# Kernel tuning notes

Measured on AMD Instinct MI355X. Metric: run time of the kernel, lower is better.

The kernel has to match this reference:

```python
import jax, jax.numpy as jnp
import numpy as np
import math

D_MODEL = 1024
NUM_HEADS = 16
D_K = D_MODEL // NUM_HEADS
B, S = 2, 2048


def _linear_weight(key, out_f, in_f):
    return jax.random.normal(key, (out_f, in_f), jnp.float32) * math.sqrt(2.0 / in_f)


def setup_inputs() -> dict:
    key = jax.random.key(0)
    ks = jax.random.split(key, 5)
    x = jax.random.normal(ks[0], (B, S, D_MODEL), jnp.float32)
    return {
        "x": x,
        "Wq": _linear_weight(ks[1], D_MODEL, D_MODEL),
        "bq": jnp.zeros((D_MODEL,), jnp.float32),
        "Wk": _linear_weight(ks[2], D_MODEL, D_MODEL),
        "bk": jnp.zeros((D_MODEL,), jnp.float32),
        "Wv": _linear_weight(ks[3], D_MODEL, D_MODEL),
        "bv": jnp.zeros((D_MODEL,), jnp.float32),
        "Wo": _linear_weight(ks[4], D_MODEL, D_MODEL),
        "bo": jnp.zeros((D_MODEL,), jnp.float32),
    }


def reference(x, Wq, bq, Wk, bk, Wv, bv, Wo, bo):
    b, s, _ = x.shape
    # Projections: x @ W.T + b (CustomLinear stores weight as (out, in))
    q = jnp.einsum("bsd,ed->bse", x, Wq) + bq
    k = jnp.einsum("bsd,ed->bse", x, Wk) + bk
    v = jnp.einsum("bsd,ed->bse", x, Wv) + bv
    # (b, h, s, d_k)
    q = q.reshape(b, s, NUM_HEADS, D_K).transpose(0, 2, 1, 3)
    k = k.reshape(b, s, NUM_HEADS, D_K).transpose(0, 2, 1, 3)
    v = v.reshape(b, s, NUM_HEADS, D_K).transpose(0, 2, 1, 3)
    # Scaled dot-product attention with fully materialized scores (faithful)
    scores = jnp.einsum("bhqd,bhkd->bhqk", q, k) / math.sqrt(D_K)
    attn = jax.nn.softmax(scores, axis=-1)
    out = jnp.einsum("bhqk,bhkd->bhqd", attn, v)
    out = out.transpose(0, 2, 1, 3).reshape(b, s, D_MODEL)
    return jnp.einsum("bsd,ed->bse", out, Wo) + bo
```

## Files before the change

kernel.cpp:

```cpp
#include <hip/hip_runtime.h>
#include <hip/hip_bf16.h>

using bf16 = __hip_bfloat16;
typedef __attribute__((ext_vector_type(8))) short short8;
typedef __attribute__((ext_vector_type(4))) short s4v;
typedef __attribute__((ext_vector_type(4))) float float4v;
typedef __attribute__((ext_vector_type(4))) float f32x4;

#define MFMA16(a, b, c) __builtin_amdgcn_mfma_f32_16x16x32_bf16((a), (b), (c), 0, 0, 0)

#define GLD_LDS16(g, l)                                            \
    __builtin_amdgcn_global_load_lds(                              \
        (const __attribute__((address_space(1))) void*)(g),        \
        (__attribute__((address_space(3))) void*)(l), 16, 0, 0)

constexpr int Bc = 2;
constexpr int Sc = 2048;
constexpr int Hc = 16;
constexpr int DKc = 64;
constexpr int Dc = 1024;
constexpr size_t MEG = 1024 * 1024;

union BFU { bf16 h; short s; };

__device__ inline short bfbits(float f) {
    BFU u; u.h = __float2bfloat16(f); return u.s;
}

__device__ inline short8 load_cvt8(const float* __restrict__ p) {
    f32x4 a = *(const f32x4*)p;
    f32x4 b = *(const f32x4*)(p + 4);
    short8 r;
    r[0] = bfbits(a[0]); r[1] = bfbits(a[1]); r[2] = bfbits(a[2]); r[3] = bfbits(a[3]);
    r[4] = bfbits(b[0]); r[5] = bfbits(b[1]); r[6] = bfbits(b[2]); r[7] = bfbits(b[3]);
    return r;
}

__global__ __launch_bounds__(256) void cvt_kernel(
    const float* __restrict__ x, const float* __restrict__ Wq,
    const float* __restrict__ Wk, const float* __restrict__ Wv,
    const float* __restrict__ Wo, bf16* __restrict__ dst)
{
    const size_t i = ((size_t)blockIdx.x * 256 + threadIdx.x) * 8;
    const float* s;
    if      (i < 4 * MEG) s = x  + i;
    else if (i < 5 * MEG) s = Wq + (i - 4 * MEG);
    else if (i < 6 * MEG) s = Wk + (i - 5 * MEG);
    else if (i < 7 * MEG) s = Wv + (i - 6 * MEG);
    else                  s = Wo + (i - 7 * MEG);
    *(short8*)(dst + i) = load_cvt8(s);
}

__global__ __launch_bounds__(256) void qkv_gemm_kernel(
    const bf16* __restrict__ x,
    const bf16* __restrict__ Wq, const float* __restrict__ bq,
    const bf16* __restrict__ Wk, const float* __restrict__ bk,
    const bf16* __restrict__ Wv, const float* __restrict__ bv,
    bf16* __restrict__ q_ws, bf16* __restrict__ k_ws, bf16* __restrict__ v_ws)
{
    constexpr int BM = 128, BN = 128, BK = 32;
    __shared__ __align__(16) bf16 sA[BM * BK];
    __shared__ __align__(16) bf16 sB[BN * BK];

    const int bx = blockIdx.x;
    const int sel = bx >> 3;
    const int n0 = (bx & 7) * BN;
    const int m0 = blockIdx.y * BM;

    const bf16* __restrict__ Wsel = (sel == 0) ? Wq : ((sel == 1) ? Wk : Wv);
    const float* __restrict__ bsel = (sel == 0) ? bq : ((sel == 1) ? bk : bv);

    const int t = threadIdx.x;
    const int lane = t & 63;
    const int wave = t >> 6;
    const int ln = lane & 15;
    const int qd = lane >> 4;
    const int wm = (wave >> 1) * 64;
    const int wn = (wave & 1) * 64;

    const int gr = lane >> 2;
    const int gc = (lane & 3) * 8;

    float4v acc[4][4];
#pragma unroll
    for (int i = 0; i < 4; i++)
#pragma unroll
        for (int j = 0; j < 4; j++) acc[i][j] = (float4v)0.0f;

    for (int kk = 0; kk < Dc; kk += BK) {
        __syncthreads();
#pragma unroll
        for (int cc = 0; cc < 2; cc++) {
            const int c = wave * 2 + cc;
            GLD_LDS16(x    + (size_t)(m0 + c * 16 + gr) * Dc + kk + gc, &sA[c * 512]);
            GLD_LDS16(Wsel + (size_t)(n0 + c * 16 + gr) * Dc + kk + gc, &sB[c * 512]);
        }
        __syncthreads();

        short8 af[4], wf[4];
#pragma unroll
        for (int i = 0; i < 4; i++)
            af[i] = *(const short8*)&sA[(wm + i * 16 + ln) * BK + qd * 8];
#pragma unroll
        for (int j = 0; j < 4; j++)
            wf[j] = *(const short8*)&sB[(wn + j * 16 + ln) * BK + qd * 8];
#pragma unroll
        for (int i = 0; i < 4; i++)
#pragma unroll
            for (int j = 0; j < 4; j++)
                acc[i][j] = MFMA16(af[i], wf[j], acc[i][j]);
    }

    constexpr float QSCALE = 0.125f * 1.44269504088896f;

#pragma unroll
    for (int j = 0; j < 4; j++) {
        const int n = n0 + wn + j * 16 + ln;
        const float bias = bsel[n];
        const int h_ = n >> 6, d_ = n & 63;
#pragma unroll
        for (int i = 0; i < 4; i++) {
            const int mbase = m0 + wm + i * 16 + qd * 4;
#pragma unroll
            for (int r = 0; r < 4; r++) {
                const int m = mbase + r;
                const int b_ = m >> 11, s_ = m & 2047;
                float v = acc[i][j][r] + bias;
                if (sel == 0) v *= QSCALE;
                const bf16 o = __float2bfloat16(v);
                if (sel == 0)
                    q_ws[(((size_t)(b_ * Hc + h_)) * Sc + s_) * DKc + d_] = o;
                else if (sel == 1)
                    k_ws[(((size_t)(b_ * Hc + h_)) * Sc + s_) * DKc + d_] = o;
                else
                    v_ws[(((size_t)(b_ * Hc + h_)) * DKc + d_) * Sc + s_] = o;
            }
        }
    }
}

__global__ __launch_bounds__(256) void attn_kernel(
    const bf16* __restrict__ q_ws, const bf16* __restrict__ k_ws,
    const bf16* __restrict__ v_ws, bf16* __restrict__ ao_ws)
{
    constexpr int LQ = 72;
    constexpr int LQP = 76;
    __shared__ __align__(16) bf16 sQ[128 * LQ];
    __shared__ __align__(16) bf16 sK[64 * LQ];
    __shared__ __align__(16) bf16 sV[80 * LQ];
    __shared__ __align__(16) short sP[4][32 * LQP];

    const int bh = blockIdx.x;
    const int qt = blockIdx.y;
    const int t = threadIdx.x;
    const int lane = t & 63;
    const int wave = t >> 6;
    const int ln = lane & 15;
    const int qd = lane >> 4;

    const bf16* __restrict__ Qbase = q_ws + (size_t)bh * Sc * DKc + qt * 128 * DKc;
    const bf16* __restrict__ Kbase = k_ws + (size_t)bh * Sc * DKc;
    const bf16* __restrict__ Vbase = v_ws + (size_t)bh * DKc * Sc;

    {
        const int row = t >> 3;
        const int col = (t & 7) * 8;
#pragma unroll
        for (int rr = 0; rr < 128; rr += 32)
            *(short8*)&sQ[(row + rr) * LQ + col] =
                *(const short8*)&Qbase[(row + rr) * DKc + col];
    }
    {
        const bf16 one = __float2bfloat16(1.0f);
        const bf16 zero = __float2bfloat16(0.0f);
        for (int idx = t; idx < 16 * LQ; idx += 256) {
            const int row = 64 + idx / LQ;
            sV[row * LQ + (idx % LQ)] = (row == 64) ? one : zero;
        }
    }

    float4v oacc[2][5];
#pragma unroll
    for (int mt = 0; mt < 2; mt++)
#pragma unroll
        for (int j = 0; j < 5; j++) oacc[mt][j] = (float4v)0.0f;

    for (int kt = 0; kt < Sc / 64; kt++) {
        __syncthreads();
        {
            const int row = t >> 3;
            const int col = (t & 7) * 8;
            const bf16* ksrc = Kbase + kt * 64 * DKc;
            *(short8*)&sK[row * LQ + col]        = *(const short8*)&ksrc[row * DKc + col];
            *(short8*)&sK[(row + 32) * LQ + col] = *(const short8*)&ksrc[(row + 32) * DKc + col];
            const bf16* vsrc = Vbase + kt * 64;
            *(short8*)&sV[row * LQ + col]        = *(const short8*)&vsrc[row * Sc + col];
            *(short8*)&sV[(row + 32) * LQ + col] = *(const short8*)&vsrc[(row + 32) * Sc + col];
        }
        __syncthreads();

        float4v sacc[2][4];
#pragma unroll
        for (int mt = 0; mt < 2; mt++)
#pragma unroll
            for (int j = 0; j < 4; j++) sacc[mt][j] = (float4v)0.0f;
#pragma unroll
        for (int ks = 0; ks < 2; ks++) {
            const short8 aq0 = *(const short8*)&sQ[(wave * 32 + ln) * LQ + ks * 32 + qd * 8];
            const short8 aq1 = *(const short8*)&sQ[(wave * 32 + 16 + ln) * LQ + ks * 32 + qd * 8];
#pragma unroll
            for (int j = 0; j < 4; j++) {
                const short8 bk_ = *(const short8*)&sK[(j * 16 + ln) * LQ + ks * 32 + qd * 8];
                sacc[0][j] = MFMA16(aq0, bk_, sacc[0][j]);
                sacc[1][j] = MFMA16(aq1, bk_, sacc[1][j]);
            }
        }

#pragma unroll
        for (int mt = 0; mt < 2; mt++)
#pragma unroll
            for (int j = 0; j < 4; j++)
#pragma unroll
                for (int r = 0; r < 4; r++)
                    sP[wave][(mt * 16 + qd * 4 + r) * LQP + j * 16 + ln] =
                        bfbits(exp2f(sacc[mt][j][r]));

#pragma unroll
        for (int ks = 0; ks < 2; ks++) {
            short8 ap[2];
#pragma unroll
            for (int mt = 0; mt < 2; mt++) {
                const s4v p0 = *(const s4v*)&sP[wave][(mt * 16 + ln) * LQP + ks * 32 + qd * 8];
                const s4v p1 = *(const s4v*)&sP[wave][(mt * 16 + ln) * LQP + ks * 32 + qd * 8 + 4];
                ap[mt][0] = p0[0]; ap[mt][1] = p0[1]; ap[mt][2] = p0[2]; ap[mt][3] = p0[3];
                ap[mt][4] = p1[0]; ap[mt][5] = p1[1]; ap[mt][6] = p1[2]; ap[mt][7] = p1[3];
            }
#pragma unroll
            for (int j = 0; j < 5; j++) {
                const short8 bv_ = *(const short8*)&sV[(j * 16 + ln) * LQ + ks * 32 + qd * 8];
                oacc[0][j] = MFMA16(ap[0], bv_, oacc[0][j]);
                oacc[1][j] = MFMA16(ap[1], bv_, oacc[1][j]);
            }
        }
    }

    const int b_ = bh >> 4, h_ = bh & 15;
#pragma unroll
    for (int mt = 0; mt < 2; mt++) {
#pragma unroll
        for (int r = 0; r < 4; r++) {
            const float l = __shfl(oacc[mt][4][r], lane & 48, 64);
            const float inv = 1.0f / l;
            const int s_ = qt * 128 + wave * 32 + mt * 16 + qd * 4 + r;
#pragma unroll
            for (int j = 0; j < 4; j++) {
                const int d_ = j * 16 + ln;
                ao_ws[(((size_t)(b_ * Sc + s_)) * Hc + h_) * DKc + d_] =
                    __float2bfloat16(oacc[mt][j][r] * inv);
            }
        }
    }
}

__global__ __launch_bounds__(256) void out_gemm_kernel(
    const bf16* __restrict__ A, const bf16* __restrict__ Wo,
    const float* __restrict__ bo, float* __restrict__ out)
{
    constexpr int BM = 128, BN = 128, BK = 32;
    __shared__ __align__(16) bf16 sA[BM * BK];
    __shared__ __align__(16) bf16 sB[BN * BK];

    const int n0 = blockIdx.x * BN;
    const int m0 = blockIdx.y * BM;

    const int t = threadIdx.x;
    const int lane = t & 63;
    const int wave = t >> 6;
    const int ln = lane & 15;
    const int qd = lane >> 4;
    const int wm = (wave >> 1) * 64;
    const int wn = (wave & 1) * 64;

    const int gr = lane >> 2;
    const int gc = (lane & 3) * 8;

    float4v acc[4][4];
#pragma unroll
    for (int i = 0; i < 4; i++)
#pragma unroll
        for (int j = 0; j < 4; j++) acc[i][j] = (float4v)0.0f;

    for (int kk = 0; kk < Dc; kk += BK) {
        __syncthreads();
#pragma unroll
        for (int cc = 0; cc < 2; cc++) {
            const int c = wave * 2 + cc;
            GLD_LDS16(A  + (size_t)(m0 + c * 16 + gr) * Dc + kk + gc, &sA[c * 512]);
            GLD_LDS16(Wo + (size_t)(n0 + c * 16 + gr) * Dc + kk + gc, &sB[c * 512]);
        }
        __syncthreads();

        short8 af[4], wf[4];
#pragma unroll
        for (int i = 0; i < 4; i++)
            af[i] = *(const short8*)&sA[(wm + i * 16 + ln) * BK + qd * 8];
#pragma unroll
        for (int j = 0; j < 4; j++)
            wf[j] = *(const short8*)&sB[(wn + j * 16 + ln) * BK + qd * 8];
#pragma unroll
        for (int i = 0; i < 4; i++)
#pragma unroll
            for (int j = 0; j < 4; j++)
                acc[i][j] = MFMA16(af[i], wf[j], acc[i][j]);
    }

#pragma unroll
    for (int j = 0; j < 4; j++) {
        const int n = n0 + wn + j * 16 + ln;
        const float bias = bo[n];
#pragma unroll
        for (int i = 0; i < 4; i++) {
            const int mbase = m0 + wm + i * 16 + qd * 4;
#pragma unroll
            for (int r = 0; r < 4; r++) {
                const int m = mbase + r;
                out[(size_t)m * Dc + n] = acc[i][j][r] + bias;
            }
        }
    }
}

extern "C" void kernel_launch(void* const* d_in, const int* in_sizes, int n_in,
                              void* d_out, int out_size, void* d_ws, size_t ws_size,
                              hipStream_t stream)
{
    const float* x  = (const float*)d_in[0];
    const float* Wq = (const float*)d_in[1];
    const float* bq = (const float*)d_in[2];
    const float* Wk = (const float*)d_in[3];
    const float* bk = (const float*)d_in[4];
    const float* Wv = (const float*)d_in[5];
    const float* bv = (const float*)d_in[6];
    const float* Wo = (const float*)d_in[7];
    const float* bo = (const float*)d_in[8];
    float* out = (float*)d_out;

    bf16* base  = (bf16*)d_ws;
    bf16* q_ws  = base;
    bf16* k_ws  = base + 4 * MEG;
    bf16* v_ws  = base + 8 * MEG;
    bf16* ao_ws = base + 12 * MEG;
    bf16* xb    = base + 16 * MEG;
    bf16* wqb   = base + 20 * MEG;
    bf16* wkb   = base + 21 * MEG;
    bf16* wvb   = base + 22 * MEG;
    bf16* wob   = base + 23 * MEG;

    cvt_kernel<<<dim3(4096), 256, 0, stream>>>(x, Wq, Wk, Wv, Wo, xb);
    qkv_gemm_kernel<<<dim3(24, 32), 256, 0, stream>>>(
        xb, wqb, bq, wkb, bk, wvb, bv, q_ws, k_ws, v_ws);
    attn_kernel<<<dim3(32, 16), 256, 0, stream>>>(q_ws, k_ws, v_ws, ao_ws);
    out_gemm_kernel<<<dim3(8, 32), 256, 0, stream>>>(ao_ws, wob, bo, out);
}
```

Measured before the change: 229.6 us.

## Double GEMM K-tile to 64 and shrink attention LDS footprint for occupancy

Both projection GEMMs now stage 64-wide K slices per barrier pair instead of 32, which halves the number of sync and load rounds per tile. The attention kernel packs its LDS into one buffer and processes the P tile one 16-row M slice at a time, so each wave's P scratch is half as large. It also only writes the ones row of the V augmentation instead of zero-filling 16 rows. Total LDS drops, which should allow more resident blocks per CU. The risk is more LDS bank conflicts from the 128-byte row stride in the GEMMs, and extra serialization in attention, where P is written and read twice per tile.

New measurement: 270.8 us. 1.18x slower.

```diff
diff --git a/kernel.cpp b/kernel.cpp
--- a/kernel.cpp
+++ b/kernel.cpp
@@ -58,7 +58,7 @@
     const bf16* __restrict__ Wv, const float* __restrict__ bv,
     bf16* __restrict__ q_ws, bf16* __restrict__ k_ws, bf16* __restrict__ v_ws)
 {
-    constexpr int BM = 128, BN = 128, BK = 32;
+    constexpr int BM = 128, BN = 128, BK = 64;
     __shared__ __align__(16) bf16 sA[BM * BK];
     __shared__ __align__(16) bf16 sB[BN * BK];
 
@@ -78,8 +78,8 @@
     const int wm = (wave >> 1) * 64;
     const int wn = (wave & 1) * 64;
 
-    const int gr = lane >> 2;
-    const int gc = (lane & 3) * 8;
+    const int gr = lane >> 3;
+    const int gc = (lane & 7) * 8;
 
     float4v acc[4][4];
 #pragma unroll
@@ -90,25 +90,28 @@
     for (int kk = 0; kk < Dc; kk += BK) {
         __syncthreads();
 #pragma unroll
-        for (int cc = 0; cc < 2; cc++) {
-            const int c = wave * 2 + cc;
-            GLD_LDS16(x    + (size_t)(m0 + c * 16 + gr) * Dc + kk + gc, &sA[c * 512]);
-            GLD_LDS16(Wsel + (size_t)(n0 + c * 16 + gr) * Dc + kk + gc, &sB[c * 512]);
-        }
-        __syncthreads();
-
-        short8 af[4], wf[4];
-#pragma unroll
-        for (int i = 0; i < 4; i++)
-            af[i] = *(const short8*)&sA[(wm + i * 16 + ln) * BK + qd * 8];
-#pragma unroll
-        for (int j = 0; j < 4; j++)
-            wf[j] = *(const short8*)&sB[(wn + j * 16 + ln) * BK + qd * 8];
-#pragma unroll
-        for (int i = 0; i < 4; i++)
+        for (int cc = 0; cc < 4; cc++) {
+            const int c = wave * 4 + cc;
+            GLD_LDS16(x    + (size_t)(m0 + c * 8 + gr) * Dc + kk + gc, &sA[c * 512]);
+            GLD_LDS16(Wsel + (size_t)(n0 + c * 8 + gr) * Dc + kk + gc, &sB[c * 512]);
+        }
+        __syncthreads();
+
+#pragma unroll
+        for (int h = 0; h < 2; h++) {
+            short8 af[4], wf[4];
+#pragma unroll
+            for (int i = 0; i < 4; i++)
+                af[i] = *(const short8*)&sA[(wm + i * 16 + ln) * BK + h * 32 + qd * 8];
 #pragma unroll
             for (int j = 0; j < 4; j++)
-                acc[i][j] = MFMA16(af[i], wf[j], acc[i][j]);
+                wf[j] = *(const short8*)&sB[(wn + j * 16 + ln) * BK + h * 32 + qd * 8];
+#pragma unroll
+            for (int i = 0; i < 4; i++)
+#pragma unroll
+                for (int j = 0; j < 4; j++)
+                    acc[i][j] = MFMA16(af[i], wf[j], acc[i][j]);
+        }
     }
 
     constexpr float QSCALE = 0.125f * 1.44269504088896f;
@@ -145,10 +148,11 @@
 {
     constexpr int LQ = 72;
     constexpr int LQP = 76;
-    __shared__ __align__(16) bf16 sQ[128 * LQ];
-    __shared__ __align__(16) bf16 sK[64 * LQ];
-    __shared__ __align__(16) bf16 sV[80 * LQ];
-    __shared__ __align__(16) short sP[4][32 * LQP];
+    __shared__ __align__(16) bf16 smem[9216 + 4608 + 4680 + 4864];
+    bf16* const sQ = smem;
+    bf16* const sK = smem + 9216;
+    bf16* const sV = smem + 13824;
+    short* const sPall = (short*)(smem + 18504);
 
     const int bh = blockIdx.x;
     const int qt = blockIdx.y;
@@ -157,6 +161,7 @@
     const int wave = t >> 6;
     const int ln = lane & 15;
     const int qd = lane >> 4;
+    short* const sPw = sPall + wave * (16 * LQP);
 
     const bf16* __restrict__ Qbase = q_ws + (size_t)bh * Sc * DKc + qt * 128 * DKc;
     const bf16* __restrict__ Kbase = k_ws + (size_t)bh * Sc * DKc;
@@ -170,14 +175,7 @@
             *(short8*)&sQ[(row + rr) * LQ + col] =
                 *(const short8*)&Qbase[(row + rr) * DKc + col];
     }
-    {
-        const bf16 one = __float2bfloat16(1.0f);
-        const bf16 zero = __float2bfloat16(0.0f);
-        for (int idx = t; idx < 16 * LQ; idx += 256) {
-            const int row = 64 + idx / LQ;
-            sV[row * LQ + (idx % LQ)] = (row == 64) ? one : zero;
-        }
-    }
+    if (t < LQ) sV[64 * LQ + t] = __float2bfloat16(1.0f);
 
     float4v oacc[2][5];
 #pragma unroll
@@ -217,29 +215,25 @@
         }
 
 #pragma unroll
-        for (int mt = 0; mt < 2; mt++)
+        for (int mt = 0; mt < 2; mt++) {
 #pragma unroll
             for (int j = 0; j < 4; j++)
 #pragma unroll
                 for (int r = 0; r < 4; r++)
-                    sP[wave][(mt * 16 + qd * 4 + r) * LQP + j * 16 + ln] =
+                    sPw[(qd * 4 + r) * LQP + j * 16 + ln] =
                         bfbits(exp2f(sacc[mt][j][r]));
-
-#pragma unroll
-        for (int ks = 0; ks < 2; ks++) {
-            short8 ap[2];
-#pragma unroll
-            for (int mt = 0; mt < 2; mt++) {
-                const s4v p0 = *(const s4v*)&sP[wave][(mt * 16 + ln) * LQP + ks * 32 + qd * 8];
-                const s4v p1 = *(const s4v*)&sP[wave][(mt * 16 + ln) * LQP + ks * 32 + qd * 8 + 4];
-                ap[mt][0] = p0[0]; ap[mt][1] = p0[1]; ap[mt][2] = p0[2]; ap[mt][3] = p0[3];
-                ap[mt][4] = p1[0]; ap[mt][5] = p1[1]; ap[mt][6] = p1[2]; ap[mt][7] = p1[3];
-            }
-#pragma unroll
-            for (int j = 0; j < 5; j++) {
-                const short8 bv_ = *(const short8*)&sV[(j * 16 + ln) * LQ + ks * 32 + qd * 8];
-                oacc[0][j] = MFMA16(ap[0], bv_, oacc[0][j]);
-                oacc[1][j] = MFMA16(ap[1], bv_, oacc[1][j]);
+#pragma unroll
+            for (int ks = 0; ks < 2; ks++) {
+                const s4v p0 = *(const s4v*)&sPw[ln * LQP + ks * 32 + qd * 8];
+                const s4v p1 = *(const s4v*)&sPw[ln * LQP + ks * 32 + qd * 8 + 4];
+                short8 ap;
+                ap[0] = p0[0]; ap[1] = p0[1]; ap[2] = p0[2]; ap[3] = p0[3];
+                ap[4] = p1[0]; ap[5] = p1[1]; ap[6] = p1[2]; ap[7] = p1[3];
+#pragma unroll
+                for (int j = 0; j < 5; j++) {
+                    const short8 bv_ = *(const short8*)&sV[(j * 16 + ln) * LQ + ks * 32 + qd * 8];
+                    oacc[mt][j] = MFMA16(ap, bv_, oacc[mt][j]);
+                }
             }
         }
     }
@@ -266,7 +260,7 @@
     const bf16* __restrict__ A, const bf16* __restrict__ Wo,
     const float* __restrict__ bo, float* __restrict__ out)
 {
-    constexpr int BM = 128, BN = 128, BK = 32;
+    constexpr int BM = 128, BN = 128, BK = 64;
     __shared__ __align__(16) bf16 sA[BM * BK];
     __shared__ __align__(16) bf16 sB[BN * BK];
 
@@ -281,8 +275,8 @@
     const int wm = (wave >> 1) * 64;
     const int wn = (wave & 1) * 64;
 
-    const int gr = lane >> 2;
-    const int gc = (lane & 3) * 8;
+    const int gr = lane >> 3;
+    const int gc = (lane & 7) * 8;
 
     float4v acc[4][4];
 #pragma unroll
@@ -293,25 +287,28 @@
     for (int kk = 0; kk < Dc; kk += BK) {
         __syncthreads();
 #pragma unroll
-        for (int cc = 0; cc < 2; cc++) {
-            const int c = wave * 2 + cc;
-            GLD_LDS16(A  + (size_t)(m0 + c * 16 + gr) * Dc + kk + gc, &sA[c * 512]);
-            GLD_LDS16(Wo + (size_t)(n0 + c * 16 + gr) * Dc + kk + gc, &sB[c * 512]);
-        }
-        __syncthreads();
-
-        short8 af[4], wf[4];
-#pragma unroll
-        for (int i = 0; i < 4; i++)
-            af[i] = *(const short8*)&sA[(wm + i * 16 + ln) * BK + qd * 8];
-#pragma unroll
-        for (int j = 0; j < 4; j++)
-            wf[j] = *(const short8*)&sB[(wn + j * 16 + ln) * BK + qd * 8];
-#pragma unroll
-        for (int i = 0; i < 4; i++)
+        for (int cc = 0; cc < 4; cc++) {
+            const int c = wave * 4 + cc;
+            GLD_LDS16(A  + (size_t)(m0 + c * 8 + gr) * Dc + kk + gc, &sA[c * 512]);
+            GLD_LDS16(Wo + (size_t)(n0 + c * 8 + gr) * Dc + kk + gc, &sB[c * 512]);
+        }
+        __syncthreads();
+
+#pragma unroll
+        for (int h = 0; h < 2; h++) {
+            short8 af[4], wf[4];
+#pragma unroll
+            for (int i = 0; i < 4; i++)
+                af[i] = *(const short8*)&sA[(wm + i * 16 + ln) * BK + h * 32 + qd * 8];
 #pragma unroll
             for (int j = 0; j < 4; j++)
-                acc[i][j] = MFMA16(af[i], wf[j], acc[i][j]);
+                wf[j] = *(const short8*)&sB[(wn + j * 16 + ln) * BK + h * 32 + qd * 8];
+#pragma unroll
+            for (int i = 0; i < 4; i++)
+#pragma unroll
+                for (int j = 0; j < 4; j++)
+                    acc[i][j] = MFMA16(af[i], wf[j], acc[i][j]);
+        }
     }
 
 #pragma unroll
```

## Double-buffer K/V with async global-to-LDS loads and XOR-swizzled LDS layout

Applied to the files above, without the earlier changes.

Replaces the padded, synchronously staged Q/K/V shared-memory tiles with XOR-swizzled unpadded tiles filled by global_load_lds. K/V get two buffers so the next tile is prefetched while the current one is computed, which removes one barrier per iteration. The QK^T MFMA operands are swapped so each lane writes P as a packed 4-element vector, and the softmax row-sum now comes from a register-held ones vector instead of extra LDS rows. This relies on the barrier also waiting for outstanding async LDS loads, and the swizzle indexing has to match on every read path.

After: 214.9 us. 6.4% less time.

```diff
diff --git a/kernel.cpp b/kernel.cpp
--- a/kernel.cpp
+++ b/kernel.cpp
@@ -143,11 +143,10 @@
     const bf16* __restrict__ q_ws, const bf16* __restrict__ k_ws,
     const bf16* __restrict__ v_ws, bf16* __restrict__ ao_ws)
 {
-    constexpr int LQ = 72;
     constexpr int LQP = 76;
-    __shared__ __align__(16) bf16 sQ[128 * LQ];
-    __shared__ __align__(16) bf16 sK[64 * LQ];
-    __shared__ __align__(16) bf16 sV[80 * LQ];
+    __shared__ __align__(16) bf16 sQ[128 * 64];
+    __shared__ __align__(16) bf16 sK[2][64 * 64];
+    __shared__ __align__(16) bf16 sV[2][64 * 64];
     __shared__ __align__(16) short sP[4][32 * LQP];
 
     const int bh = blockIdx.x;
@@ -157,26 +156,40 @@
     const int wave = t >> 6;
     const int ln = lane & 15;
     const int qd = lane >> 4;
+    short* const sPw = sP[wave];
 
     const bf16* __restrict__ Qbase = q_ws + (size_t)bh * Sc * DKc + qt * 128 * DKc;
     const bf16* __restrict__ Kbase = k_ws + (size_t)bh * Sc * DKc;
     const bf16* __restrict__ Vbase = v_ws + (size_t)bh * DKc * Sc;
 
+    const int rloc = lane >> 3;
+    const int blk = lane & 7;
+
     {
-        const int row = t >> 3;
-        const int col = (t & 7) * 8;
-#pragma unroll
-        for (int rr = 0; rr < 128; rr += 32)
-            *(short8*)&sQ[(row + rr) * LQ + col] =
-                *(const short8*)&Qbase[(row + rr) * DKc + col];
+#pragma unroll
+        for (int cc = 0; cc < 4; cc++) {
+            const int c = wave * 4 + cc;
+            const int row = c * 8 + rloc;
+            const int gb = blk ^ (row & 7);
+            GLD_LDS16(Qbase + (size_t)row * DKc + gb * 8, &sQ[c * 512]);
+        }
     }
     {
-        const bf16 one = __float2bfloat16(1.0f);
-        const bf16 zero = __float2bfloat16(0.0f);
-        for (int idx = t; idx < 16 * LQ; idx += 256) {
-            const int row = 64 + idx / LQ;
-            sV[row * LQ + (idx % LQ)] = (row == 64) ? one : zero;
-        }
+#pragma unroll
+        for (int cc = 0; cc < 2; cc++) {
+            const int c = wave * 2 + cc;
+            const int row = c * 8 + rloc;
+            const int gb = blk ^ (row & 7);
+            GLD_LDS16(Kbase + (size_t)row * DKc + gb * 8, &sK[0][c * 512]);
+            GLD_LDS16(Vbase + (size_t)row * Sc + gb * 8, &sV[0][c * 512]);
+        }
+    }
+
+    short8 ones8;
+    {
+        const short ob = (ln == 0) ? (short)0x3F80 : (short)0;
+#pragma unroll
+        for (int i = 0; i < 8; i++) ones8[i] = ob;
     }
 
     float4v oacc[2][5];
@@ -186,18 +199,21 @@
         for (int j = 0; j < 5; j++) oacc[mt][j] = (float4v)0.0f;
 
     for (int kt = 0; kt < Sc / 64; kt++) {
-        __syncthreads();
-        {
-            const int row = t >> 3;
-            const int col = (t & 7) * 8;
-            const bf16* ksrc = Kbase + kt * 64 * DKc;
-            *(short8*)&sK[row * LQ + col]        = *(const short8*)&ksrc[row * DKc + col];
-            *(short8*)&sK[(row + 32) * LQ + col] = *(const short8*)&ksrc[(row + 32) * DKc + col];
-            const bf16* vsrc = Vbase + kt * 64;
-            *(short8*)&sV[row * LQ + col]        = *(const short8*)&vsrc[row * Sc + col];
-            *(short8*)&sV[(row + 32) * LQ + col] = *(const short8*)&vsrc[(row + 32) * Sc + col];
-        }
-        __syncthreads();
+        const int cur = kt & 1;
+        __syncthreads();
+        if (kt + 1 < Sc / 64) {
+            const int nxt = (kt + 1) & 1;
+#pragma unroll
+            for (int cc = 0; cc < 2; cc++) {
+                const int c = wave * 2 + cc;
+                const int row = c * 8 + rloc;
+                const int gb = blk ^ (row & 7);
+                GLD_LDS16(Kbase + (size_t)((kt + 1) * 64 + row) * DKc + gb * 8,
+                          &sK[nxt][c * 512]);
+                GLD_LDS16(Vbase + (size_t)row * Sc + (kt + 1) * 64 + gb * 8,
+                          &sV[nxt][c * 512]);
+            }
+        }
 
         float4v sacc[2][4];
 #pragma unroll
@@ -206,41 +222,54 @@
             for (int j = 0; j < 4; j++) sacc[mt][j] = (float4v)0.0f;
 #pragma unroll
         for (int ks = 0; ks < 2; ks++) {
-            const short8 aq0 = *(const short8*)&sQ[(wave * 32 + ln) * LQ + ks * 32 + qd * 8];
-            const short8 aq1 = *(const short8*)&sQ[(wave * 32 + 16 + ln) * LQ + ks * 32 + qd * 8];
+            short8 bq[2];
+#pragma unroll
+            for (int mt = 0; mt < 2; mt++) {
+                const int row = wave * 32 + mt * 16 + ln;
+                bq[mt] = *(const short8*)
+                    &sQ[row * 64 + (((ks * 4 + qd) ^ (row & 7)) << 3)];
+            }
 #pragma unroll
             for (int j = 0; j < 4; j++) {
-                const short8 bk_ = *(const short8*)&sK[(j * 16 + ln) * LQ + ks * 32 + qd * 8];
-                sacc[0][j] = MFMA16(aq0, bk_, sacc[0][j]);
-                sacc[1][j] = MFMA16(aq1, bk_, sacc[1][j]);
+                const int row = j * 16 + ln;
+                const short8 ak = *(const short8*)
+                    &sK[cur][row * 64 + (((ks * 4 + qd) ^ (row & 7)) << 3)];
+                sacc[0][j] = MFMA16(ak, bq[0], sacc[0][j]);
+                sacc[1][j] = MFMA16(ak, bq[1], sacc[1][j]);
             }
         }
 
 #pragma unroll
         for (int mt = 0; mt < 2; mt++)
 #pragma unroll
-            for (int j = 0; j < 4; j++)
+            for (int j = 0; j < 4; j++) {
+                s4v pk;
 #pragma unroll
                 for (int r = 0; r < 4; r++)
-                    sP[wave][(mt * 16 + qd * 4 + r) * LQP + j * 16 + ln] =
-                        bfbits(exp2f(sacc[mt][j][r]));
+                    pk[r] = bfbits(exp2f(sacc[mt][j][r]));
+                *(s4v*)&sPw[(mt * 16 + ln) * LQP + j * 16 + qd * 4] = pk;
+            }
 
 #pragma unroll
         for (int ks = 0; ks < 2; ks++) {
             short8 ap[2];
 #pragma unroll
             for (int mt = 0; mt < 2; mt++) {
-                const s4v p0 = *(const s4v*)&sP[wave][(mt * 16 + ln) * LQP + ks * 32 + qd * 8];
-                const s4v p1 = *(const s4v*)&sP[wave][(mt * 16 + ln) * LQP + ks * 32 + qd * 8 + 4];
+                const s4v p0 = *(const s4v*)&sPw[(mt * 16 + ln) * LQP + ks * 32 + qd * 8];
+                const s4v p1 = *(const s4v*)&sPw[(mt * 16 + ln) * LQP + ks * 32 + qd * 8 + 4];
                 ap[mt][0] = p0[0]; ap[mt][1] = p0[1]; ap[mt][2] = p0[2]; ap[mt][3] = p0[3];
                 ap[mt][4] = p1[0]; ap[mt][5] = p1[1]; ap[mt][6] = p1[2]; ap[mt][7] = p1[3];
             }
 #pragma unroll
-            for (int j = 0; j < 5; j++) {
-                const short8 bv_ = *(const short8*)&sV[(j * 16 + ln) * LQ + ks * 32 + qd * 8];
+            for (int j = 0; j < 4; j++) {
+                const int row = j * 16 + ln;
+                const short8 bv_ = *(const short8*)
+                    &sV[cur][row * 64 + (((ks * 4 + qd) ^ (row & 7)) << 3)];
                 oacc[0][j] = MFMA16(ap[0], bv_, oacc[0][j]);
                 oacc[1][j] = MFMA16(ap[1], bv_, oacc[1][j]);
             }
+            oacc[0][4] = MFMA16(ap[0], ones8, oacc[0][4]);
+            oacc[1][4] = MFMA16(ap[1], ones8, oacc[1][4]);
         }
     }
 
```
